# Kernel tuning notes

Measured on AMD Instinct MI355X. Metric: run time of the kernel, lower is better.

Reference implementation:

```python
import jax, jax.numpy as jnp
import numpy as np

N_NODES = 50000
N_EDGES = 1200000
N_REL = 45
IN_C, HID_C, OUT_C = 64, 32, 16


def setup_inputs() -> dict:
    key = jax.random.key(0)
    ks = jax.random.split(key, 9)
    x = jax.random.normal(ks[0], (N_NODES, IN_C), dtype=jnp.float32)
    edge_index = jax.random.randint(ks[1], (2, N_EDGES), 0, N_NODES, dtype=jnp.int64)
    edge_type = jax.random.randint(ks[2], (N_EDGES,), 0, N_REL, dtype=jnp.int64)
    s = 0.05
    W1 = jax.random.normal(ks[3], (N_REL, IN_C, HID_C), dtype=jnp.float32) * s
    root1 = jax.random.normal(ks[4], (IN_C, HID_C), dtype=jnp.float32) * s
    b1 = jax.random.normal(ks[5], (HID_C,), dtype=jnp.float32) * s
    W2 = jax.random.normal(ks[6], (N_REL, HID_C, OUT_C), dtype=jnp.float32) * s
    root2 = jax.random.normal(ks[7], (HID_C, OUT_C), dtype=jnp.float32) * s
    b2 = jax.random.normal(ks[8], (OUT_C,), dtype=jnp.float32) * s
    return {"x": x, "edge_index": edge_index, "edge_type": edge_type,
            "W1": W1, "root1": root1, "b1": b1,
            "W2": W2, "root2": root2, "b2": b2}


def rgcn_conv(x, edge_index, edge_type, W, root, b):
    # PyG RGCNConv: out_i = x_i @ root + b + sum_r mean_{j in N_r(i)} (x_j @ W_r)
    N = x.shape[0]
    R = W.shape[0]
    src, dst = edge_index[0], edge_index[1]
    # per-relation transform of all nodes: [R, N, out]
    h = jnp.einsum('ni,rio->rno', x, W)
    # per-edge message: gather transformed src feature for edge's relation
    msg = h[edge_type, src]                      # [E, out]
    # segment id combines (relation, dst) for per-relation mean aggregation
    seg = edge_type * N + dst                    # [E]
    sums = jax.ops.segment_sum(msg, seg, num_segments=R * N)        # [R*N, out]
    cnt = jax.ops.segment_sum(jnp.ones((msg.shape[0],), x.dtype), seg,
                              num_segments=R * N)                   # [R*N]
    mean = sums / jnp.maximum(cnt, 1.0)[:, None]
    agg = mean.reshape(R, N, -1).sum(axis=0)     # sum over relations -> [N, out]
    return agg + x @ root + b


def reference(x, edge_index, edge_type, W1, root1, b1, W2, root2, b2):
    h = rgcn_conv(x, edge_index, edge_type, W1, root1, b1)
    h = jax.nn.relu(h)
    out = rgcn_conv(h, edge_index, edge_type, W2, root2, b2)
    return out
```

## Files before the change

kernel.cpp:

```cpp
#include <hip/hip_runtime.h>
#include <hip/hip_fp16.h>
#include <cstdint>
#include <cstddef>

#define NN   50000
#define NE   1200000
#define NR   45
#define INC  64
#define HIDC 32
#define OUTC 16
#define MAXE 1202880
#define NCHUNK (MAXE/64)
#define EPB 4096
#define NB  ((NE + EPB - 1) / EPB)
#define QDW 6250
#define QDD 12500
#define NTILE ((NN + 255) / 256)


typedef _Float16 f16x8 __attribute__((ext_vector_type(8)));
typedef float    f32x4 __attribute__((ext_vector_type(4)));

union F16Bits { unsigned short u; _Float16 f; };
union ABFrag   { uint4 u; f16x8 f; };

__global__ __launch_bounds__(256) void preph_k(const float* __restrict__ W1,
                                               const float* __restrict__ W2,
                                               const float* __restrict__ x,
                                               const int* __restrict__ ei,
                                               const int* __restrict__ et,
                                               const float* __restrict__ root1,
                                               const float* __restrict__ root2,
                                               const float* __restrict__ b1,
                                               __half* __restrict__ W1f,
                                               __half* __restrict__ W2f,
                                               __half* __restrict__ xh,
                                               float2* __restrict__ rootp1,
                                               float2* __restrict__ rootp2,
                                               float2* __restrict__ b1p,
                                               unsigned* __restrict__ ghist,
                                               unsigned* __restrict__ rsorted,
                                               unsigned* __restrict__ flagbuf) {
    __shared__ unsigned lh[4 * 48];
    int t = threadIdx.x, b = blockIdx.x;
    int wv = t >> 6;
    if (t < 192) lh[t] = 0;
    __syncthreads();
    if (b < NB) {
        #pragma unroll
        for (int it = 0; it < EPB / 256; ++it) {
            int e = b * EPB + it * 256 + t;
            if (e < NE) {
                int r = et[e], src = ei[e], dst = ei[NE + e];
                if ((unsigned)r < NR && (unsigned)src < NN && (unsigned)dst < NN)
                    atomicAdd(&lh[wv * 48 + r], 1u);
            }
        }
    }
    __syncthreads();
    if (b < NB && t < NR)
        ghist[t * NB + b] = lh[t] + lh[48 + t] + lh[96 + t] + lh[144 + t];
    int g = b * 256 + t;
    int gthreads = gridDim.x * 256;
    for (int i = g; i < MAXE; i += gthreads) rsorted[i] = 0xFFFFFFFFu;
    if (b == 0) flagbuf[t] = 0;
    if (g < NR * 2048) {
        int r = g >> 11, rem = g & 2047;
        int kb = rem >> 10, nb = (rem >> 9) & 1;
        int lane = (rem >> 3) & 63, j = rem & 7;
        int k = kb * 32 + (lane >> 4) * 8 + j;
        int n = nb * 16 + (lane & 15);
        W1f[g] = __float2half(W1[(r * INC + k) * HIDC + n]);
    }
    if (g < NR * 512) {
        int r = g >> 9, rem = g & 511;
        int lane = (rem >> 3) & 63, j = rem & 7;
        int k = (lane >> 4) * 8 + j;
        int kc = (k >> 1) + ((k & 1) << 4);
        int n = lane & 15;
        W2f[g] = __float2half(W2[(r * HIDC + kc) * OUTC + n]);
    }
    if (g < NN * INC / 2) {
        float2 f = ((const float2*)x)[g];
        union { __half2 h; unsigned u; } cv;
        cv.h = __floats2half2_rn(f.x, f.y);
        ((unsigned*)xh)[g] = cv.u;
    }
    if (g < 1024) {
        int in = g >> 4, w = g & 15;
        rootp1[g] = make_float2(root1[in * HIDC + w], root1[in * HIDC + w + 16]);
    }
    if (g < 256) {
        int in = g >> 3, w = g & 7;
        rootp2[g] = make_float2(root2[in * OUTC + w], root2[in * OUTC + w + 8]);
    }
    if (g < 16) b1p[g] = make_float2(b1[g], b1[g + 16]);
}

__global__ __launch_bounds__(1024) void scat_k(const int* __restrict__ ei,
                                               const int* __restrict__ et,
                                               const unsigned* __restrict__ ghist,
                                               unsigned* __restrict__ rngs,
                                               int* __restrict__ chunkrel,
                                               unsigned* __restrict__ rsorted) {
    __shared__ unsigned reltot[NR];
    __shared__ unsigned mypart[NR];
    __shared__ unsigned relbase[NR + 1];
    __shared__ unsigned lbase[NR], lcur[NR];
    int t = threadIdx.x, bx = blockIdx.x;
    if (t < NR) {
        unsigned total = 0, part = 0;
        const unsigned* __restrict__ row = ghist + t * NB;
        for (int b = 0; b < NB; ++b) {
            if (b == bx) part = total;
            total += row[b];
        }
        reltot[t] = total;
        mypart[t] = part;
        lcur[t] = 0;
    }
    __syncthreads();
    if (t == 0) {
        unsigned acc = 0;
        for (int r = 0; r < NR; ++r) {
            relbase[r] = acc;
            acc += ((reltot[r] + 63u) >> 6) << 6;
        }
        relbase[NR] = acc;
    }
    __syncthreads();
    if (t < NR) lbase[t] = relbase[t] + mypart[t];
    __syncthreads();
    #pragma unroll
    for (int it = 0; it < EPB / 1024; ++it) {
        int e = bx * EPB + it * 1024 + t;
        if (e < NE) {
            int r = et[e], src = ei[e], dst = ei[NE + e];
            if ((unsigned)r < NR && (unsigned)src < NN && (unsigned)dst < NN) {
                unsigned local = atomicAdd(&lcur[r], 1u);
                rsorted[lbase[r] + local] = (unsigned)src | ((unsigned)dst << 16);
            }
        }
    }
    if (bx == 0) {
        if (t < NR) {
            rngs[2 * t]     = relbase[t];
            rngs[2 * t + 1] = relbase[t] + reltot[t];
        }
        for (int c = t; c < NCHUNK; c += 1024) {
            unsigned pos = (unsigned)c << 6;
            int lo = 0, hi = NR - 1;
            while (lo < hi) {
                int mid = (lo + hi + 1) >> 1;
                if (relbase[mid] <= pos) lo = mid; else hi = mid - 1;
            }
            chunkrel[c] = lo;
        }
    }
}

__global__ __launch_bounds__(1024) void relcnt_k(const unsigned* __restrict__ rsorted,
                                                 const unsigned* __restrict__ rngs,
                                                 unsigned short* __restrict__ cnt16,
                                                 unsigned short* __restrict__ rank16) {
    __shared__ unsigned lds[QDW];
    int r = blockIdx.x >> 2, q = blockIdx.x & 3, t = threadIdx.x;
    unsigned base = rngs[2 * r], end = rngs[2 * r + 1];
    unsigned dlo = q * QDD, dhi = dlo + QDD;
    for (int w = t; w < QDW; w += 1024) lds[w] = 0;
    __syncthreads();
    for (unsigned s = base + t; s < end; s += 1024) {
        unsigned d = rsorted[s] >> 16;
        if (d >= dlo && d < dhi) {
            unsigned off = d - dlo;
            unsigned old = atomicAdd(&lds[off >> 1], (off & 1) ? 0x10000u : 1u);
            rank16[s] = (unsigned short)((off & 1) ? (old >> 16) : (old & 0xFFFFu));
        }
    }
    __syncthreads();
    unsigned* __restrict__ cp = (unsigned*)(cnt16 + (size_t)r * NN + dlo);
    for (int w = t; w < QDW; w += 1024) cp[w] = lds[w];
}

__global__ __launch_bounds__(256) void dp_k(const unsigned short* __restrict__ cnt16,
                                            unsigned* __restrict__ packed,
                                            unsigned* __restrict__ rowptr,
                                            unsigned* __restrict__ flags) {
    __shared__ unsigned wsum[4];
    __shared__ unsigned excl_s;
    int t = threadIdx.x, b = blockIdx.x;
    int lane = t & 63, wv = t >> 6;
    int dst = b * 256 + t;
    unsigned deg = 0;
    if (dst < NN) {
        unsigned run = 0;
        #pragma unroll 5
        for (int r = 0; r < NR; ++r) {
            unsigned c = cnt16[(size_t)r * NN + dst];
            F16Bits fb; fb.f = (_Float16)(c ? 1.0f / (float)c : 0.0f);
            packed[(size_t)r * NN + dst] = (run & 0xFFFFu) | ((unsigned)fb.u << 16);
            run += c;
        }
        deg = run;
    }
    unsigned s = deg;
    #pragma unroll
    for (int off = 1; off < 64; off <<= 1) {
        unsigned n = __shfl_up(s, off);
        if (lane >= off) s += n;
    }
    if (lane == 63) wsum[wv] = s;
    __syncthreads();
    unsigned waveoff = 0;
    if (wv > 0) waveoff += wsum[0];
    if (wv > 1) waveoff += wsum[1];
    if (wv > 2) waveoff += wsum[2];
    unsigned blockT = wsum[0] + wsum[1] + wsum[2] + wsum[3];
    unsigned local_excl = waveoff + s - deg;
    if (t == 0) {
        if (b == 0) {
            excl_s = 0;
            atomicExch(&flags[0], 0x80000000u | blockT);
        } else {
            atomicExch(&flags[b], 0x40000000u | blockT);
            unsigned ex = 0;
            int p = b - 1;
            while (p >= 0) {
                unsigned f = atomicAdd(&flags[p], 0u);
                unsigned st = f >> 30;
                if (st == 0) continue;
                ex += f & 0x3FFFFFFFu;
                if (st >= 2) break;
                --p;
            }
            excl_s = ex;
            atomicExch(&flags[b], 0x80000000u | (ex + blockT));
        }
    }
    __syncthreads();
    unsigned ex = excl_s;
    if (dst < NN) rowptr[dst] = ex + local_excl;
    if (b == (int)gridDim.x - 1 && t == 0) rowptr[NN] = ex + blockT;
}

__global__ __launch_bounds__(256) void finalize_k(const unsigned* __restrict__ rsorted,
                                                  const unsigned short* __restrict__ rank16,
                                                  const unsigned* __restrict__ packed,
                                                  const unsigned* __restrict__ rowptr,
                                                  const int* __restrict__ chunkrel,
                                                  uint2* __restrict__ pedges) {
    int s = blockIdx.x * 256 + threadIdx.x;
    if (s >= MAXE) return;
    unsigned v = rsorted[s];
    unsigned dst = v >> 16;
    if (dst >= NN) { pedges[s] = make_uint2(0u, 0x80000000u); return; }
    int r = chunkrel[s >> 6];
    unsigned pk = packed[(size_t)r * NN + dst];
    unsigned dpos = rowptr[dst] + (pk & 0xFFFFu) + (unsigned)rank16[s];
    pedges[s] = make_uint2((v & 0xFFFFu) | (pk & 0xFFFF0000u),
                           dpos | ((unsigned)r << 25));
}

__global__ __launch_bounds__(256) void msg1_k(const __half* __restrict__ xh,
                                              const __half* __restrict__ W1f,
                                              const uint2* __restrict__ pedges,
                                              __half* __restrict__ msg) {
    int tid = threadIdx.x;
    int lane = tid & 63;
    int wave = (blockIdx.x * 256 + tid) >> 6;
    if (wave >= NCHUNK) return;
    int e = (wave << 6) + lane;
    uint2 er = pedges[e];
    int w1 = (int)er.y;
    int rel = __builtin_amdgcn_readfirstlane((w1 >> 25) & 63);
    F16Bits fb; fb.u = (unsigned short)(er.x >> 16);
    float sc = (float)fb.f;
    int src = er.x & 0xFFFF;
    int drow = (w1 < 0) ? NE : (w1 & 0x1FFFFFF);
    const uint4* __restrict__ wf = (const uint4*)W1f + (size_t)rel * 256;
    ABFrag b00, b01, b10, b11;
    b00.u = wf[0 * 64 + lane];
    b01.u = wf[1 * 64 + lane];
    b10.u = wf[2 * 64 + lane];
    b11.u = wf[3 * 64 + lane];
    int quad = lane >> 4, col = lane & 15;
    ABFrag a0[4], a1[4];
    #pragma unroll
    for (int tl = 0; tl < 4; ++tl) {
        int s = __shfl(src, tl * 16 + col);
        const uint4* __restrict__ xp = (const uint4*)(xh + (size_t)s * INC) + quad;
        a0[tl].u = xp[0];
        a1[tl].u = xp[4];
    }
    #pragma unroll
    for (int tl = 0; tl < 4; ++tl) {
        f32x4 acc0 = {0.f, 0.f, 0.f, 0.f}, acc1 = {0.f, 0.f, 0.f, 0.f};
        acc0 = __builtin_amdgcn_mfma_f32_16x16x32_f16(a0[tl].f, b00.f, acc0, 0, 0, 0);
        acc0 = __builtin_amdgcn_mfma_f32_16x16x32_f16(a1[tl].f, b10.f, acc0, 0, 0, 0);
        acc1 = __builtin_amdgcn_mfma_f32_16x16x32_f16(a0[tl].f, b01.f, acc1, 0, 0, 0);
        acc1 = __builtin_amdgcn_mfma_f32_16x16x32_f16(a1[tl].f, b11.f, acc1, 0, 0, 0);
        #pragma unroll
        for (int i = 0; i < 4; ++i) {
            int ee = tl * 16 + quad * 4 + i;
            int dr   = __shfl(drow, ee);
            float si = __shfl(sc, ee);
            union { __half2 h; unsigned u; } cv;
            cv.h = __floats2half2_rn(acc0[i] * si, acc1[i] * si);
            ((unsigned*)(msg + (size_t)dr * HIDC))[col] = cv.u;
        }
    }
}

__global__ __launch_bounds__(256) void msg2_k(const __half* __restrict__ hh,
                                              const __half* __restrict__ W2f,
                                              const uint2* __restrict__ pedges,
                                              __half* __restrict__ msg) {
    int tid = threadIdx.x;
    int lane = tid & 63;
    int wave = (blockIdx.x * 256 + tid) >> 6;
    if (wave >= NCHUNK) return;
    int e = (wave << 6) + lane;
    uint2 er = pedges[e];
    int w1 = (int)er.y;
    int rel = __builtin_amdgcn_readfirstlane((w1 >> 25) & 63);
    F16Bits fb; fb.u = (unsigned short)(er.x >> 16);
    float sc = (float)fb.f;
    int src = er.x & 0xFFFF;
    int drow = (w1 < 0) ? NE : (w1 & 0x1FFFFFF);
    ABFrag bf;
    bf.u = ((const uint4*)W2f + (size_t)rel * 64)[lane];
    int quad = lane >> 4, col = lane & 15;
    ABFrag a[4];
    #pragma unroll
    for (int tl = 0; tl < 4; ++tl) {
        int s = __shfl(src, tl * 16 + col);
        a[tl].u = *((const uint4*)(hh + (size_t)s * HIDC) + quad);
    }
    #pragma unroll
    for (int tl = 0; tl < 4; ++tl) {
        f32x4 acc = {0.f, 0.f, 0.f, 0.f};
        acc = __builtin_amdgcn_mfma_f32_16x16x32_f16(a[tl].f, bf.f, acc, 0, 0, 0);
        #pragma unroll
        for (int i = 0; i < 4; ++i) {
            int ee = tl * 16 + quad * 4 + i;
            int dr   = __shfl(drow, ee);
            float si = __shfl(sc, ee);
            float v  = acc[i] * si;
            float p  = __shfl_xor(v, 8);
            if (col < 8) {
                union { __half2 h; unsigned u; } cv;
                cv.h = __floats2half2_rn(v, p);
                ((unsigned*)(msg + (size_t)dr * OUTC))[col] = cv.u;
            }
        }
    }
}

__global__ __launch_bounds__(256) void gather1_k(const __half* __restrict__ xh,
                                                 const float2* __restrict__ rootp1,
                                                 const float2* __restrict__ b1p,
                                                 const __half* __restrict__ msg,
                                                 const unsigned* __restrict__ rowptr,
                                                 __half* __restrict__ hh) {
    int tid = threadIdx.x;
    int lane = tid & 63;
    int wid = (blockIdx.x * 256 + tid) >> 6;
    int g = lane >> 2, j = lane & 3;
    unsigned k0 = rowptr[wid], k1 = rowptr[wid + 1];
    float2 rw[4][4];
    #pragma unroll
    for (int i = 0; i < 4; ++i) {
        const float4* __restrict__ rp =
            (const float4*)rootp1 + ((4 * g + i) << 3) + 2 * j;
        float4 u0 = rp[0], u1 = rp[1];
        rw[i][0] = make_float2(u0.x, u0.y);
        rw[i][1] = make_float2(u0.z, u0.w);
        rw[i][2] = make_float2(u1.x, u1.y);
        rw[i][3] = make_float2(u1.z, u1.w);
    }
    float acc[8] = {0.f, 0.f, 0.f, 0.f, 0.f, 0.f, 0.f, 0.f};
    for (unsigned k = k0 + g; k < k1; k += 16) {
        uint4 v = ((const uint4*)(msg + (size_t)k * HIDC))[j];
        union { unsigned u; __half2 h; } c0, c1, c2, c3;
        c0.u = v.x; c1.u = v.y; c2.u = v.z; c3.u = v.w;
        float2 f0 = __half22float2(c0.h), f1 = __half22float2(c1.h);
        float2 f2 = __half22float2(c2.h), f3 = __half22float2(c3.h);
        acc[0] += f0.x; acc[1] += f0.y;
        acc[2] += f1.x; acc[3] += f1.y;
        acc[4] += f2.x; acc[5] += f2.y;
        acc[6] += f3.x; acc[7] += f3.y;
    }
    union { uint2 u; __half2 h[2]; } xv;
    xv.u = ((const uint2*)(xh + (size_t)wid * INC))[g];
    float2 xa = __half22float2(xv.h[0]), xb = __half22float2(xv.h[1]);
    float xs[4] = { xa.x, xa.y, xb.x, xb.y };
    #pragma unroll
    for (int i = 0; i < 4; ++i) {
        #pragma unroll
        for (int q = 0; q < 4; ++q) {
            acc[2 * q]     = fmaf(xs[i], rw[i][q].x, acc[2 * q]);
            acc[2 * q + 1] = fmaf(xs[i], rw[i][q].y, acc[2 * q + 1]);
        }
    }
    #pragma unroll
    for (int off = 4; off < 64; off <<= 1) {
        #pragma unroll
        for (int q = 0; q < 8; ++q) acc[q] += __shfl_xor(acc[q], off);
    }
    if (g == 0) {
        const float4* __restrict__ bp4 = (const float4*)b1p;
        float4 bb0 = bp4[2 * j], bb1 = bp4[2 * j + 1];
        float2 bq[4] = { make_float2(bb0.x, bb0.y), make_float2(bb0.z, bb0.w),
                         make_float2(bb1.x, bb1.y), make_float2(bb1.z, bb1.w) };
        unsigned um[4];
        #pragma unroll
        for (int q = 0; q < 4; ++q) {
            float vx = acc[2 * q] + bq[q].x, vy = acc[2 * q + 1] + bq[q].y;
            union { __half2 h2; unsigned u; } cv;
            cv.h2 = __floats2half2_rn(vx > 0.f ? vx : 0.f, vy > 0.f ? vy : 0.f);
            um[q] = cv.u;
        }
        ((uint4*)(hh + (size_t)wid * HIDC))[j] = make_uint4(um[0], um[1], um[2], um[3]);
    }
}

__global__ __launch_bounds__(256) void gather2_k(const __half* __restrict__ hh,
                                                 const float2* __restrict__ rootp2,
                                                 const float* __restrict__ b2,
                                                 const __half* __restrict__ msg,
                                                 const unsigned* __restrict__ rowptr,
                                                 float* __restrict__ out) {
    int tid = threadIdx.x;
    int lane = tid & 63;
    int wid = (blockIdx.x * 256 + tid) >> 6;
    int g = lane >> 1, j = lane & 1;
    unsigned k0 = rowptr[wid], k1 = rowptr[wid + 1];
    const float4* __restrict__ rp = (const float4*)rootp2 + (g << 2) + 2 * j;
    float4 u0 = rp[0], u1 = rp[1];
    float2 rw[4] = { make_float2(u0.x, u0.y), make_float2(u0.z, u0.w),
                     make_float2(u1.x, u1.y), make_float2(u1.z, u1.w) };
    float acc[8] = {0.f, 0.f, 0.f, 0.f, 0.f, 0.f, 0.f, 0.f};
    for (unsigned k = k0 + g; k < k1; k += 32) {
        uint4 v = ((const uint4*)(msg + (size_t)k * OUTC))[j];
        union { unsigned u; __half2 h; } c0, c1, c2, c3;
        c0.u = v.x; c1.u = v.y; c2.u = v.z; c3.u = v.w;
        float2 f0 = __half22float2(c0.h), f1 = __half22float2(c1.h);
        float2 f2 = __half22float2(c2.h), f3 = __half22float2(c3.h);
        acc[0] += f0.x; acc[1] += f0.y;
        acc[2] += f1.x; acc[3] += f1.y;
        acc[4] += f2.x; acc[5] += f2.y;
        acc[6] += f3.x; acc[7] += f3.y;
    }
    unsigned hw = ((const unsigned*)(hh + (size_t)wid * HIDC))[g & 15];
    union { unsigned u; __half2 h; } hc; hc.u = hw;
    float2 hf = __half22float2(hc.h);
    float hv = (g < 16) ? hf.x : hf.y;
    #pragma unroll
    for (int q = 0; q < 4; ++q) {
        acc[2 * q]     = fmaf(hv, rw[q].x, acc[2 * q]);
        acc[2 * q + 1] = fmaf(hv, rw[q].y, acc[2 * q + 1]);
    }
    #pragma unroll
    for (int off = 2; off < 64; off <<= 1) {
        #pragma unroll
        for (int q = 0; q < 8; ++q) acc[q] += __shfl_xor(acc[q], off);
    }
    if (g == 0) {
        float* __restrict__ orow = out + (size_t)wid * OUTC;
        float4 ba = ((const float4*)b2)[j];
        float4 bb = ((const float4*)b2)[j + 2];
        ((float4*)orow)[j] = make_float4(acc[0] + ba.x, acc[2] + ba.y,
                                         acc[4] + ba.z, acc[6] + ba.w);
        ((float4*)orow)[j + 2] = make_float4(acc[1] + bb.x, acc[3] + bb.y,
                                             acc[5] + bb.z, acc[7] + bb.w);
    }
}

extern "C" void kernel_launch(void* const* d_in, const int* in_sizes, int n_in,
                              void* d_out, int out_size, void* d_ws, size_t ws_size,
                              hipStream_t stream) {
    const float* x     = (const float*)d_in[0];
    const int*   ei    = (const int*)d_in[1];
    const int*   et    = (const int*)d_in[2];
    const float* W1    = (const float*)d_in[3];
    const float* root1 = (const float*)d_in[4];
    const float* b1    = (const float*)d_in[5];
    const float* W2    = (const float*)d_in[6];
    const float* root2 = (const float*)d_in[7];
    const float* b2    = (const float*)d_in[8];
    float* out = (float*)d_out;

    char* ws = (char*)d_ws;
    size_t o = 0;
    auto alloc = [&](size_t bytes) -> char* {
        char* p = ws + o;
        o = (o + bytes + 255) & ~(size_t)255;
        return p;
    };
    unsigned* rsorted = (unsigned*)alloc((size_t)MAXE * 4);
    unsigned* flagbuf = (unsigned*)alloc(256 * 4);
    unsigned* ghist   = (unsigned*)alloc((size_t)NR * NB * 4);
    unsigned* rngs    = (unsigned*)alloc((size_t)NR * 2 * 4);
    int*      chunkrel= (int*)     alloc((size_t)NCHUNK * 4);
    unsigned short* rank16 = (unsigned short*)alloc((size_t)MAXE * 2);
    unsigned short* cnt16  = (unsigned short*)alloc((size_t)NR * NN * 2);
    unsigned* packed  = (unsigned*)alloc((size_t)NR * NN * 4);
    unsigned* rowptr  = (unsigned*)alloc(((size_t)NN + 1) * 4);
    uint2*    pedges  = (uint2*)   alloc((size_t)MAXE * 8);
    __half*   W1f     = (__half*)  alloc((size_t)NR * 2048 * 2);
    __half*   W2f     = (__half*)  alloc((size_t)NR * 512 * 2);
    __half*   xh      = (__half*)  alloc((size_t)NN * INC * 2);
    __half*   hh      = (__half*)  alloc((size_t)NN * HIDC * 2);
    float2*   rootp1  = (float2*)  alloc(1024 * 8);
    float2*   rootp2  = (float2*)  alloc(256 * 8);
    float2*   b1p     = (float2*)  alloc(16 * 8);
    char*     msgraw  = alloc(((size_t)NE + 1) * 64);
    __half*   msg1    = (__half*)msgraw;
    __half*   msg2    = (__half*)msgraw;

    int prep_grid = NN * INC / 2 / 256;
    preph_k   <<<prep_grid, 256, 0, stream>>>(W1, W2, x, ei, et, root1, root2, b1,
                                              W1f, W2f, xh, rootp1, rootp2, b1p,
                                              ghist, rsorted, flagbuf);
    scat_k    <<<NB, 1024, 0, stream>>>(ei, et, ghist, rngs, chunkrel, rsorted);
    relcnt_k  <<<4 * NR, 1024, 0, stream>>>(rsorted, rngs, cnt16, rank16);
    dp_k      <<<NTILE, 256, 0, stream>>>(cnt16, packed, rowptr, flagbuf + 32);
    finalize_k<<<(MAXE + 255) / 256, 256, 0, stream>>>(rsorted, rank16, packed,
                                                       rowptr, chunkrel, pedges);
    msg1_k    <<<(MAXE + 255) / 256, 256, 0, stream>>>(xh, W1f, pedges, msg1);
    gather1_k <<<NN * 64 / 256, 256, 0, stream>>>(xh, rootp1, b1p, msg1, rowptr, hh);
    msg2_k    <<<(MAXE + 255) / 256, 256, 0, stream>>>(hh, W2f, pedges, msg2);
    gather2_k <<<NN * 64 / 256, 256, 0, stream>>>(hh, rootp2, b2, msg2, rowptr, out);
}
```

Measured before the change: 294.0 us.

## Bucket edges by source-node segment within each relation for gather locality

Edges are now sorted into buckets keyed by (source node block of 4096, relation) instead of only by relation, so later message kernels gather source features from a narrower node range and get better cache hits. The per-block histogram prefix sums, previously recomputed serially in every scatter block, move into two dedicated scan kernels. This adds two kernel launches and more padding (each bucket is padded to 64). relcnt_k now loops over the 13 source segments of each relation.

```diff
diff --git a/kernel.cpp b/kernel.cpp
--- a/kernel.cpp
+++ b/kernel.cpp
@@ -9,8 +9,10 @@
 #define INC  64
 #define HIDC 32
 #define OUTC 16
-#define MAXE 1202880
-#define NCHUNK (MAXE/64)
+#define NSG  13
+#define NBKT (NSG * NR)
+#define MAXE (NE + NBKT * 64)
+#define NCHUNK (MAXE / 64)
 #define EPB 4096
 #define NB  ((NE + EPB - 1) / EPB)
 #define QDW 6250
@@ -41,10 +43,9 @@
                                                unsigned* __restrict__ ghist,
                                                unsigned* __restrict__ rsorted,
                                                unsigned* __restrict__ flagbuf) {
-    __shared__ unsigned lh[4 * 48];
+    __shared__ unsigned lh[NBKT];
     int t = threadIdx.x, b = blockIdx.x;
-    int wv = t >> 6;
-    if (t < 192) lh[t] = 0;
+    for (int i = t; i < NBKT; i += 256) lh[i] = 0;
     __syncthreads();
     if (b < NB) {
         #pragma unroll
@@ -53,13 +54,13 @@
             if (e < NE) {
                 int r = et[e], src = ei[e], dst = ei[NE + e];
                 if ((unsigned)r < NR && (unsigned)src < NN && (unsigned)dst < NN)
-                    atomicAdd(&lh[wv * 48 + r], 1u);
+                    atomicAdd(&lh[(src >> 12) * NR + r], 1u);
             }
         }
     }
     __syncthreads();
-    if (b < NB && t < NR)
-        ghist[t * NB + b] = lh[t] + lh[48 + t] + lh[96 + t] + lh[144 + t];
+    if (b < NB)
+        for (int i = t; i < NBKT; i += 256) ghist[(size_t)i * NB + b] = lh[i];
     int g = b * 256 + t;
     int gthreads = gridDim.x * 256;
     for (int i = g; i < MAXE; i += gthreads) rsorted[i] = 0xFFFFFFFFu;
@@ -97,39 +98,75 @@
     if (g < 16) b1p[g] = make_float2(b1[g], b1[g + 16]);
 }
 
+__global__ __launch_bounds__(64) void scanA_k(const unsigned* __restrict__ ghist,
+                                              unsigned* __restrict__ bbase,
+                                              unsigned* __restrict__ btot) {
+    int b = blockIdx.x, j = threadIdx.x;
+    const unsigned* __restrict__ row = ghist + (size_t)b * NB;
+    unsigned* __restrict__ orow = bbase + (size_t)b * NB;
+    unsigned v[5], s = 0;
+    #pragma unroll
+    for (int k = 0; k < 5; ++k) {
+        int idx = j * 5 + k;
+        v[k] = (idx < NB) ? row[idx] : 0u;
+        s += v[k];
+    }
+    unsigned inc = s;
+    #pragma unroll
+    for (int off = 1; off < 64; off <<= 1) {
+        unsigned n = __shfl_up(inc, off);
+        if (j >= off) inc += n;
+    }
+    unsigned run = inc - s;
+    #pragma unroll
+    for (int k = 0; k < 5; ++k) {
+        int idx = j * 5 + k;
+        if (idx < NB) orow[idx] = run;
+        run += v[k];
+    }
+    if (j == 63) btot[b] = inc;
+}
+
+__global__ __launch_bounds__(1024) void scanB_k(const unsigned* __restrict__ btot,
+                                                unsigned* __restrict__ gbase,
+                                                int* __restrict__ chunkrel) {
+    __shared__ unsigned tot[NBKT];
+    __shared__ unsigned gb[NBKT + 1];
+    int t = threadIdx.x;
+    for (int i = t; i < NBKT; i += 1024) tot[i] = btot[i];
+    __syncthreads();
+    if (t == 0) {
+        unsigned acc = 0;
+        for (int i = 0; i < NBKT; ++i) {
+            gb[i] = acc;
+            acc += (tot[i] + 63u) & ~63u;
+        }
+        gb[NBKT] = acc;
+    }
+    __syncthreads();
+    for (int i = t; i <= NBKT; i += 1024) gbase[i] = gb[i];
+    for (int c = t; c < NCHUNK; c += 1024) {
+        unsigned pos = (unsigned)c << 6;
+        int lo = 0, hi = NBKT - 1;
+        while (lo < hi) {
+            int mid = (lo + hi + 1) >> 1;
+            if (gb[mid] <= pos) lo = mid; else hi = mid - 1;
+        }
+        chunkrel[c] = lo % NR;
+    }
+}
+
 __global__ __launch_bounds__(1024) void scat_k(const int* __restrict__ ei,
                                                const int* __restrict__ et,
-                                               const unsigned* __restrict__ ghist,
-                                               unsigned* __restrict__ rngs,
-                                               int* __restrict__ chunkrel,
+                                               const unsigned* __restrict__ bbase,
+                                               const unsigned* __restrict__ gbase,
                                                unsigned* __restrict__ rsorted) {
-    __shared__ unsigned reltot[NR];
-    __shared__ unsigned mypart[NR];
-    __shared__ unsigned relbase[NR + 1];
-    __shared__ unsigned lbase[NR], lcur[NR];
+    __shared__ unsigned lbase[NBKT], lcur[NBKT];
     int t = threadIdx.x, bx = blockIdx.x;
-    if (t < NR) {
-        unsigned total = 0, part = 0;
-        const unsigned* __restrict__ row = ghist + t * NB;
-        for (int b = 0; b < NB; ++b) {
-            if (b == bx) part = total;
-            total += row[b];
-        }
-        reltot[t] = total;
-        mypart[t] = part;
-        lcur[t] = 0;
-    }
-    __syncthreads();
-    if (t == 0) {
-        unsigned acc = 0;
-        for (int r = 0; r < NR; ++r) {
-            relbase[r] = acc;
-            acc += ((reltot[r] + 63u) >> 6) << 6;
-        }
-        relbase[NR] = acc;
-    }
-    __syncthreads();
-    if (t < NR) lbase[t] = relbase[t] + mypart[t];
+    for (int i = t; i < NBKT; i += 1024) {
+        lbase[i] = gbase[i] + bbase[(size_t)i * NB + bx];
+        lcur[i] = 0;
+    }
     __syncthreads();
     #pragma unroll
     for (int it = 0; it < EPB / 1024; ++it) {
@@ -137,44 +174,32 @@
         if (e < NE) {
             int r = et[e], src = ei[e], dst = ei[NE + e];
             if ((unsigned)r < NR && (unsigned)src < NN && (unsigned)dst < NN) {
-                unsigned local = atomicAdd(&lcur[r], 1u);
-                rsorted[lbase[r] + local] = (unsigned)src | ((unsigned)dst << 16);
+                int bkt = (src >> 12) * NR + r;
+                unsigned local = atomicAdd(&lcur[bkt], 1u);
+                rsorted[lbase[bkt] + local] = (unsigned)src | ((unsigned)dst << 16);
             }
         }
     }
-    if (bx == 0) {
-        if (t < NR) {
-            rngs[2 * t]     = relbase[t];
-            rngs[2 * t + 1] = relbase[t] + reltot[t];
-        }
-        for (int c = t; c < NCHUNK; c += 1024) {
-            unsigned pos = (unsigned)c << 6;
-            int lo = 0, hi = NR - 1;
-            while (lo < hi) {
-                int mid = (lo + hi + 1) >> 1;
-                if (relbase[mid] <= pos) lo = mid; else hi = mid - 1;
-            }
-            chunkrel[c] = lo;
-        }
-    }
 }
 
 __global__ __launch_bounds__(1024) void relcnt_k(const unsigned* __restrict__ rsorted,
-                                                 const unsigned* __restrict__ rngs,
+                                                 const unsigned* __restrict__ gbase,
                                                  unsigned short* __restrict__ cnt16,
                                                  unsigned short* __restrict__ rank16) {
     __shared__ unsigned lds[QDW];
     int r = blockIdx.x >> 2, q = blockIdx.x & 3, t = threadIdx.x;
-    unsigned base = rngs[2 * r], end = rngs[2 * r + 1];
     unsigned dlo = q * QDD, dhi = dlo + QDD;
     for (int w = t; w < QDW; w += 1024) lds[w] = 0;
     __syncthreads();
-    for (unsigned s = base + t; s < end; s += 1024) {
-        unsigned d = rsorted[s] >> 16;
-        if (d >= dlo && d < dhi) {
-            unsigned off = d - dlo;
-            unsigned old = atomicAdd(&lds[off >> 1], (off & 1) ? 0x10000u : 1u);
-            rank16[s] = (unsigned short)((off & 1) ? (old >> 16) : (old & 0xFFFFu));
+    for (int sg = 0; sg < NSG; ++sg) {
+        unsigned base = gbase[sg * NR + r], end = gbase[sg * NR + r + 1];
+        for (unsigned s = base + t; s < end; s += 1024) {
+            unsigned d = rsorted[s] >> 16;
+            if (d >= dlo && d < dhi) {
+                unsigned off = d - dlo;
+                unsigned old = atomicAdd(&lds[off >> 1], (off & 1) ? 0x10000u : 1u);
+                rank16[s] = (unsigned short)((off & 1) ? (old >> 16) : (old & 0xFFFFu));
+            }
         }
     }
     __syncthreads();
@@ -499,8 +524,10 @@
     };
     unsigned* rsorted = (unsigned*)alloc((size_t)MAXE * 4);
     unsigned* flagbuf = (unsigned*)alloc(256 * 4);
-    unsigned* ghist   = (unsigned*)alloc((size_t)NR * NB * 4);
-    unsigned* rngs    = (unsigned*)alloc((size_t)NR * 2 * 4);
+    unsigned* ghist   = (unsigned*)alloc((size_t)NBKT * NB * 4);
+    unsigned* bbase   = (unsigned*)alloc((size_t)NBKT * NB * 4);
+    unsigned* btot    = (unsigned*)alloc((size_t)NBKT * 4);
+    unsigned* gbase   = (unsigned*)alloc((size_t)(NBKT + 1) * 4);
     int*      chunkrel= (int*)     alloc((size_t)NCHUNK * 4);
     unsigned short* rank16 = (unsigned short*)alloc((size_t)MAXE * 2);
     unsigned short* cnt16  = (unsigned short*)alloc((size_t)NR * NN * 2);
@@ -522,8 +549,10 @@
     preph_k   <<<prep_grid, 256, 0, stream>>>(W1, W2, x, ei, et, root1, root2, b1,
                                               W1f, W2f, xh, rootp1, rootp2, b1p,
                                               ghist, rsorted, flagbuf);
-    scat_k    <<<NB, 1024, 0, stream>>>(ei, et, ghist, rngs, chunkrel, rsorted);
-    relcnt_k  <<<4 * NR, 1024, 0, stream>>>(rsorted, rngs, cnt16, rank16);
+    scanA_k   <<<NBKT, 64, 0, stream>>>(ghist, bbase, btot);
+    scanB_k   <<<1, 1024, 0, stream>>>(btot, gbase, chunkrel);
+    scat_k    <<<NB, 1024, 0, stream>>>(ei, et, bbase, gbase, rsorted);
+    relcnt_k  <<<4 * NR, 1024, 0, stream>>>(rsorted, gbase, cnt16, rank16);
     dp_k      <<<NTILE, 256, 0, stream>>>(cnt16, packed, rowptr, flagbuf + 32);
     finalize_k<<<(MAXE + 255) / 256, 256, 0, stream>>>(rsorted, rank16, packed,
                                                        rowptr, chunkrel, pedges);
```

After: 296.7 us. No clear change (+0.9%).
